# Optimization experiments

Hardware: AMD Instinct MI355X
Metric: run time of the kernel (lower is better)

The kernel has to match this reference:

```python
import jax, jax.numpy as jnp
import numpy as np

B = 131072          # points on manifold
A = 16              # n_anchors
SDIM = 512          # substrate.n (spatial dim); ambient dim = SDIM + 1
ALPHA = 0.1         # attraction coefficient
EPS = 1e-7


def _proj(p):
    # Project onto hyperboloid: recompute time coord from spatial part.
    sp = p[..., 1:]
    t = jnp.sqrt(1.0 + jnp.sum(sp * sp, axis=-1, keepdims=True))
    return jnp.concatenate([t, sp], axis=-1)


def _linner(x, y):
    # Lorentz inner product <x,y>_L = -x0*y0 + sum_i xi*yi
    return -x[..., 0] * y[..., 0] + jnp.sum(x[..., 1:] * y[..., 1:], axis=-1)


def setup_inputs() -> dict:
    key = jax.random.key(0)
    k1, k2 = jax.random.split(key)
    x_sp = jax.random.normal(k1, (B, SDIM), dtype=jnp.float32)
    x = _proj(jnp.concatenate([jnp.zeros((B, 1), jnp.float32), x_sp], axis=-1))
    a_sp = jax.random.normal(k2, (A, SDIM), dtype=jnp.float32) * 0.01
    anchors = _proj(jnp.concatenate([jnp.zeros((A, 1), jnp.float32), a_sp], axis=-1))
    return {"x": x, "anchors": anchors}


def reference(x, anchors):
    af = _proj(anchors)                                   # [A, D]
    D = af.shape[-1]
    metric = jnp.concatenate([-jnp.ones((1,), x.dtype), jnp.ones((D - 1,), x.dtype)])
    # pairwise -<x,a>_L  -> [B, A]
    theta_all = -jnp.einsum('bd,ad->ba', x * metric, af)
    dists = jnp.arccosh(jnp.clip(theta_all, 1.0 + EPS, None))
    idx = jnp.argmin(dists, axis=1)                       # nearest anchor per point
    y = af[idx]                                           # [B, D]
    # log_map_x(y) = acosh(theta)/sqrt(theta^2-1) * (y - theta*x)
    theta = jnp.clip(-_linner(x, y), 1.0 + EPS, None)[:, None]
    direction = (jnp.arccosh(theta) / jnp.sqrt(theta * theta - 1.0)) * (y - theta * x)
    v = ALPHA * direction                                 # tangent vector
    # exp_map_x(v) = cosh(||v||_L) x + sinh(||v||_L)/||v||_L * v
    vn = jnp.sqrt(jnp.clip(_linner(v, v), EPS, None))[:, None]
    return jnp.cosh(vn) * x + (jnp.sinh(vn) / vn) * v
```

## Files before the change

kernel.cpp:

```cpp
#include <hip/hip_runtime.h>

#define NA 16
#define DD 513
#define ALPHA 0.1f
#define EPSV 1e-7f
#define TPW 4
#define GRID 1024

typedef __fp16 h2v __attribute__((ext_vector_type(2)));
typedef __fp16 f16x8 __attribute__((ext_vector_type(8)));
typedef float f32x4 __attribute__((ext_vector_type(4)));
typedef float f32x4u __attribute__((ext_vector_type(4), aligned(4)));
typedef unsigned int u32;

union H2U { h2v h; u32 u; };
union FU  { float f; u32 u; int i; };
union FRAG { u32 w[4]; f16x8 v; };
union U4   { uint4 v; u32 w[4]; };

static __device__ __forceinline__ u32 pkrtz(float lo, float hi) {
    H2U t; t.h = __builtin_amdgcn_cvt_pkrtz(lo, hi); return t.u;
}
static __device__ __forceinline__ h2v asH2(u32 w) { H2U t; t.u = w; return t.h; }

struct __attribute__((packed, aligned(4))) F4 { float x, y, z, w; };


__global__ __launch_bounds__(256, 3)
void hfield_kernel(const float* __restrict__ x,
                   const float* __restrict__ anc,
                   float* __restrict__ out) {
    __shared__ uint4 bframe[NA * 64];
    __shared__ uint4 xframe[4][8 * 64];

    const int tid = threadIdx.x, lane = tid & 63, wid = tid >> 6;
    const int col = lane & 15, g = lane >> 4;

    const int rowbase0 = (blockIdx.x * 4 + wid) * (8 * TPW);
    const float* xb = x + (size_t)rowbase0 * DD;
    uint4* xf = xframe[wid];

    F4 nvA[8], nvB[8];
#pragma unroll
    for (int r = 0; r < 8; ++r) {
        const float* p = xb + (size_t)r * DD + 1 + 4 * lane;
        nvA[r] = *(const F4*)p;
        nvB[r] = *(const F4*)(p + 256);
    }
    __builtin_amdgcn_sched_barrier(0);

#pragma unroll
    for (int m = 0; m < 4; ++m) {
        const int i = m * 256 + tid;
        const int a = i >> 6, u = i & 63;
        const float* p = anc + a * DD + 1 + 4 * u;
        const float* q = p + 256;
        uint4 w;
        w.x = pkrtz(p[0], p[1]);
        w.y = pkrtz(p[2], p[3]);
        w.z = pkrtz(q[0], q[1]);
        w.w = pkrtz(q[2], q[3]);
        bframe[a * 64 + (u ^ (a & 7))] = w;
    }

    float af0c;
    {
        const float* p = anc + col * DD + 1 + g * 128;
        float s = 0.f;
#pragma unroll 16
        for (int i = 0; i < 128; ++i) s = fmaf(p[i], p[i], s);
        s += __shfl_xor(s, 16);
        s += __shfl_xor(s, 32);
        af0c = sqrtf(1.0f + s);
    }
    __syncthreads();

    const float thmin = 1.0f + 1e-7f;

#pragma unroll 1
    for (int t = 0; t < TPW; ++t) {
        const int rowbase = rowbase0 + t * 8;

#pragma unroll
        for (int r = 0; r < 8; ++r) {
            uint4 w;
            w.x = pkrtz(nvA[r].x, nvA[r].y);
            w.y = pkrtz(nvA[r].z, nvA[r].w);
            w.z = pkrtz(nvB[r].x, nvB[r].y);
            w.w = pkrtz(nvB[r].z, nvB[r].w);
            xf[r * 64 + (lane ^ (r & 7))] = w;
        }

        if (t + 1 < TPW) {
            const float* nb = xb + (size_t)((t + 1) * 8) * DD;
#pragma unroll
            for (int r = 0; r < 8; ++r) {
                const float* p = nb + (size_t)r * DD + 1 + 4 * lane;
                nvA[r] = *(const F4*)p;
                nvB[r] = *(const F4*)(p + 256);
            }
            __builtin_amdgcn_sched_barrier(0);
        }

        float x0r[4];
#pragma unroll
        for (int r4 = 0; r4 < 4; ++r4)
            x0r[r4] = xb[(size_t)(t * 8 + ((4 * g + r4) & 7)) * DD];

        f32x4 acc = {0.f, 0.f, 0.f, 0.f};
#pragma unroll
        for (int kt = 0; kt < 16; ++kt) {
            const int u = 4 * kt + g;
            FRAG A, B;
            U4 ax, bx;
            ax.v = xf[(col & 7) * 64 + (u ^ (col & 7))];
            bx.v = bframe[col * 64 + (u ^ (col & 7))];
            A.w[0] = ax.w[0]; A.w[1] = ax.w[1]; A.w[2] = ax.w[2]; A.w[3] = ax.w[3];
            B.w[0] = bx.w[0]; B.w[1] = bx.w[1]; B.w[2] = bx.w[2]; B.w[3] = bx.w[3];
            acc = __builtin_amdgcn_mfma_f32_16x16x32_f16(A.v, B.v, acc, 0, 0, 0);
        }

        float c1r[4], c2r[4], o0r[4];
        int bir[4];
#pragma unroll
        for (int r4 = 0; r4 < 4; ++r4) {
            const float th = fmaxf(fmaf(x0r[r4], af0c, -acc[r4]), thmin);
            FU u; u.f = th;
            u32 key = (u.u & 0xFFFFFFF0u) | (u32)col;
#pragma unroll
            for (int m = 1; m <= 8; m <<= 1) {
                const u32 o = (u32)__shfl_xor((int)key, m);
                key = o < key ? o : key;
            }
            const int bi  = (int)(key & 15u);
            const int src = (lane & 48) | bi;
            const float thw = __shfl(th, src);
            const float y0  = __shfl(af0c, src);

            const float s2 = thw * thw - 1.0f;
            const float rr = sqrtf(s2);
            const float ac = __logf(thw + rr);
            const float cf = ac / rr;
            const float vn = sqrtf(fmaxf(ALPHA * ALPHA * ac * ac, EPSV));
            const float e  = __expf(vn);
            const float ei = 1.0f / e;
            const float ch = 0.5f * (e + ei);
            const float sh = 0.5f * (e - ei);
            const float c2 = ALPHA * cf * (sh / vn);
            const float c1 = fmaf(-c2, thw, ch);

            c1r[r4] = c1;
            c2r[r4] = c2;
            o0r[r4] = fmaf(c2, y0, c1 * x0r[r4]);
            bir[r4] = bi;
        }

#pragma unroll
        for (int r = 0; r < 8; ++r) {
            const int src = (r >> 2) * 16;
            const float c1 = __shfl(c1r[r & 3], src);
            const float c2 = __shfl(c2r[r & 3], src);
            const float o0 = __shfl(o0r[r & 3], src);
            const int   bi = __builtin_amdgcn_readfirstlane(__shfl(bir[r & 3], src));

            U4 X, Y;
            X.v = xf[r * 64 + (lane ^ (r & 7))];
            Y.v = bframe[bi * 64 + (lane ^ (bi & 7))];

            f32x4u s0, s1;
#pragma unroll
            for (int q = 0; q < 2; ++q) {
                const h2v hx = asH2(X.w[q]);
                const h2v hy = asH2(Y.w[q]);
                s0[2 * q]     = fmaf(c2, (float)hy.x, c1 * (float)hx.x);
                s0[2 * q + 1] = fmaf(c2, (float)hy.y, c1 * (float)hx.y);
            }
#pragma unroll
            for (int q = 0; q < 2; ++q) {
                const h2v hx = asH2(X.w[2 + q]);
                const h2v hy = asH2(Y.w[2 + q]);
                s1[2 * q]     = fmaf(c2, (float)hy.x, c1 * (float)hx.x);
                s1[2 * q + 1] = fmaf(c2, (float)hy.y, c1 * (float)hx.y);
            }
            float* op = out + (size_t)(rowbase + r) * DD;
            __builtin_nontemporal_store(s0, (f32x4u*)(op + 1 + 4 * lane));
            __builtin_nontemporal_store(s1, (f32x4u*)(op + 257 + 4 * lane));
            if (lane == 0) __builtin_nontemporal_store(o0, op);
        }
    }
}

extern "C" void kernel_launch(void* const* d_in, const int* in_sizes, int n_in,
                              void* d_out, int out_size, void* d_ws, size_t ws_size,
                              hipStream_t stream) {
    const float* x   = (const float*)d_in[0];
    const float* anc = (const float*)d_in[1];
    float* out       = (float*)d_out;
    hipLaunchKernelGGL(hfield_kernel, dim3(GRID), dim3(256), 0, stream, x, anc, out);
}
```

Baseline: 103.9 us.

## Use FP8 MFMA for anchor distances and keep x in fp16 registers

Switches the x·anchor dot product from fp16 16x16x32 MFMA to fp8 MFMA, storing both x and the anchors (anchors pre-scaled by 16) as packed fp8 in LDS, which halves LDS footprint and read traffic. The output combine now reads x from fp16 values held in registers and the anchor from fp8 LDS. Occupancy hint rises from 3 to 4 blocks, and the next-tile prefetch moves after the output stores, which reduces overlap of loads with compute. FP8 lowers accuracy in both argmin selection and the output's anchor term, so nearest-anchor choices may differ and tolerances may be exceeded.

```diff
diff --git a/kernel.cpp b/kernel.cpp
--- a/kernel.cpp
+++ b/kernel.cpp
@@ -8,37 +8,41 @@
 #define GRID 1024
 
 typedef __fp16 h2v __attribute__((ext_vector_type(2)));
-typedef __fp16 f16x8 __attribute__((ext_vector_type(8)));
+typedef float f32x2 __attribute__((ext_vector_type(2)));
 typedef float f32x4 __attribute__((ext_vector_type(4)));
 typedef float f32x4u __attribute__((ext_vector_type(4), aligned(4)));
 typedef unsigned int u32;
 
 union H2U { h2v h; u32 u; };
 union FU  { float f; u32 u; int i; };
-union FRAG { u32 w[4]; f16x8 v; };
-union U4   { uint4 v; u32 w[4]; };
+union U2L { uint2 v; long l; };
 
 static __device__ __forceinline__ u32 pkrtz(float lo, float hi) {
     H2U t; t.h = __builtin_amdgcn_cvt_pkrtz(lo, hi); return t.u;
 }
 static __device__ __forceinline__ h2v asH2(u32 w) { H2U t; t.u = w; return t.h; }
+static __device__ __forceinline__ u32 pk8(float a, float b, float c, float d) {
+    int w = __builtin_amdgcn_cvt_pk_fp8_f32(a, b, 0, false);
+    w = __builtin_amdgcn_cvt_pk_fp8_f32(c, d, w, true);
+    return (u32)w;
+}
 
 struct __attribute__((packed, aligned(4))) F4 { float x, y, z, w; };
 
 
-__global__ __launch_bounds__(256, 3)
+__global__ __launch_bounds__(256, 4)
 void hfield_kernel(const float* __restrict__ x,
                    const float* __restrict__ anc,
                    float* __restrict__ out) {
-    __shared__ uint4 bframe[NA * 64];
-    __shared__ uint4 xframe[4][8 * 64];
+    __shared__ uint2 bframe[NA * 64];
+    __shared__ uint2 xframe[4][8 * 64];
 
     const int tid = threadIdx.x, lane = tid & 63, wid = tid >> 6;
     const int col = lane & 15, g = lane >> 4;
 
     const int rowbase0 = (blockIdx.x * 4 + wid) * (8 * TPW);
     const float* xb = x + (size_t)rowbase0 * DD;
-    uint4* xf = xframe[wid];
+    uint2* xf = xframe[wid];
 
     F4 nvA[8], nvB[8];
 #pragma unroll
@@ -52,15 +56,13 @@
 #pragma unroll
     for (int m = 0; m < 4; ++m) {
         const int i = m * 256 + tid;
-        const int a = i >> 6, u = i & 63;
-        const float* p = anc + a * DD + 1 + 4 * u;
-        const float* q = p + 256;
-        uint4 w;
-        w.x = pkrtz(p[0], p[1]);
-        w.y = pkrtz(p[2], p[3]);
-        w.z = pkrtz(q[0], q[1]);
-        w.w = pkrtz(q[2], q[3]);
-        bframe[a * 64 + (u ^ (a & 7))] = w;
+        const int a = i >> 6, p = i & 63;
+        const float* s = anc + a * DD + 1 + 4 * p;
+        const float* q = s + 256;
+        uint2 w;
+        w.x = pk8(s[0] * 16.f, s[1] * 16.f, s[2] * 16.f, s[3] * 16.f);
+        w.y = pk8(q[0] * 16.f, q[1] * 16.f, q[2] * 16.f, q[3] * 16.f);
+        bframe[a * 64 + (p ^ a)] = w;
     }
 
     float af0c;
@@ -81,25 +83,17 @@
     for (int t = 0; t < TPW; ++t) {
         const int rowbase = rowbase0 + t * 8;
 
+        u32 xq[8][4];
 #pragma unroll
         for (int r = 0; r < 8; ++r) {
-            uint4 w;
-            w.x = pkrtz(nvA[r].x, nvA[r].y);
-            w.y = pkrtz(nvA[r].z, nvA[r].w);
-            w.z = pkrtz(nvB[r].x, nvB[r].y);
-            w.w = pkrtz(nvB[r].z, nvB[r].w);
-            xf[r * 64 + (lane ^ (r & 7))] = w;
-        }
-
-        if (t + 1 < TPW) {
-            const float* nb = xb + (size_t)((t + 1) * 8) * DD;
-#pragma unroll
-            for (int r = 0; r < 8; ++r) {
-                const float* p = nb + (size_t)r * DD + 1 + 4 * lane;
-                nvA[r] = *(const F4*)p;
-                nvB[r] = *(const F4*)(p + 256);
-            }
-            __builtin_amdgcn_sched_barrier(0);
+            uint2 w;
+            w.x = pk8(nvA[r].x, nvA[r].y, nvA[r].z, nvA[r].w);
+            w.y = pk8(nvB[r].x, nvB[r].y, nvB[r].z, nvB[r].w);
+            xf[r * 64 + (lane ^ (2 * r))] = w;
+            xq[r][0] = pkrtz(nvA[r].x, nvA[r].y);
+            xq[r][1] = pkrtz(nvA[r].z, nvA[r].w);
+            xq[r][2] = pkrtz(nvB[r].x, nvB[r].y);
+            xq[r][3] = pkrtz(nvB[r].z, nvB[r].w);
         }
 
         float x0r[4];
@@ -110,21 +104,18 @@
         f32x4 acc = {0.f, 0.f, 0.f, 0.f};
 #pragma unroll
         for (int kt = 0; kt < 16; ++kt) {
-            const int u = 4 * kt + g;
-            FRAG A, B;
-            U4 ax, bx;
-            ax.v = xf[(col & 7) * 64 + (u ^ (col & 7))];
-            bx.v = bframe[col * 64 + (u ^ (col & 7))];
-            A.w[0] = ax.w[0]; A.w[1] = ax.w[1]; A.w[2] = ax.w[2]; A.w[3] = ax.w[3];
-            B.w[0] = bx.w[0]; B.w[1] = bx.w[1]; B.w[2] = bx.w[2]; B.w[3] = bx.w[3];
-            acc = __builtin_amdgcn_mfma_f32_16x16x32_f16(A.v, B.v, acc, 0, 0, 0);
+            const int p = 4 * kt + g;
+            U2L A, B;
+            A.v = xf[(col & 7) * 64 + (p ^ (2 * (col & 7)))];
+            B.v = bframe[col * 64 + (p ^ col)];
+            acc = __builtin_amdgcn_mfma_f32_16x16x32_fp8_fp8(A.l, B.l, acc, 0, 0, 0);
         }
 
         float c1r[4], c2r[4], o0r[4];
         int bir[4];
 #pragma unroll
         for (int r4 = 0; r4 < 4; ++r4) {
-            const float th = fmaxf(fmaf(x0r[r4], af0c, -acc[r4]), thmin);
+            const float th = fmaxf(fmaf(x0r[r4], af0c, -acc[r4] * 0.0625f), thmin);
             FU u; u.f = th;
             u32 key = (u.u & 0xFFFFFFF0u) | (u32)col;
 #pragma unroll
@@ -162,30 +153,43 @@
             const float c2 = __shfl(c2r[r & 3], src);
             const float o0 = __shfl(o0r[r & 3], src);
             const int   bi = __builtin_amdgcn_readfirstlane(__shfl(bir[r & 3], src));
-
-            U4 X, Y;
-            X.v = xf[r * 64 + (lane ^ (r & 7))];
-            Y.v = bframe[bi * 64 + (lane ^ (bi & 7))];
+            const float c2s = c2 * 0.0625f;
+
+            const uint2 yw = bframe[bi * 64 + (lane ^ bi)];
+            const f32x2 ylo0 = __builtin_amdgcn_cvt_pk_f32_fp8((int)yw.x, false);
+            const f32x2 ylo1 = __builtin_amdgcn_cvt_pk_f32_fp8((int)yw.x, true);
+            const f32x2 yhi0 = __builtin_amdgcn_cvt_pk_f32_fp8((int)yw.y, false);
+            const f32x2 yhi1 = __builtin_amdgcn_cvt_pk_f32_fp8((int)yw.y, true);
+
+            const h2v xa = asH2(xq[r][0]);
+            const h2v xb2 = asH2(xq[r][1]);
+            const h2v xc = asH2(xq[r][2]);
+            const h2v xd = asH2(xq[r][3]);
 
             f32x4u s0, s1;
-#pragma unroll
-            for (int q = 0; q < 2; ++q) {
-                const h2v hx = asH2(X.w[q]);
-                const h2v hy = asH2(Y.w[q]);
-                s0[2 * q]     = fmaf(c2, (float)hy.x, c1 * (float)hx.x);
-                s0[2 * q + 1] = fmaf(c2, (float)hy.y, c1 * (float)hx.y);
-            }
-#pragma unroll
-            for (int q = 0; q < 2; ++q) {
-                const h2v hx = asH2(X.w[2 + q]);
-                const h2v hy = asH2(Y.w[2 + q]);
-                s1[2 * q]     = fmaf(c2, (float)hy.x, c1 * (float)hx.x);
-                s1[2 * q + 1] = fmaf(c2, (float)hy.y, c1 * (float)hx.y);
-            }
+            s0[0] = fmaf(c2s, ylo0.x, c1 * (float)xa.x);
+            s0[1] = fmaf(c2s, ylo0.y, c1 * (float)xa.y);
+            s0[2] = fmaf(c2s, ylo1.x, c1 * (float)xb2.x);
+            s0[3] = fmaf(c2s, ylo1.y, c1 * (float)xb2.y);
+            s1[0] = fmaf(c2s, yhi0.x, c1 * (float)xc.x);
+            s1[1] = fmaf(c2s, yhi0.y, c1 * (float)xc.y);
+            s1[2] = fmaf(c2s, yhi1.x, c1 * (float)xd.x);
+            s1[3] = fmaf(c2s, yhi1.y, c1 * (float)xd.y);
+
             float* op = out + (size_t)(rowbase + r) * DD;
             __builtin_nontemporal_store(s0, (f32x4u*)(op + 1 + 4 * lane));
             __builtin_nontemporal_store(s1, (f32x4u*)(op + 257 + 4 * lane));
             if (lane == 0) __builtin_nontemporal_store(o0, op);
+        }
+
+        if (t + 1 < TPW) {
+            const float* nb = xb + (size_t)((t + 1) * 8) * DD;
+#pragma unroll
+            for (int r = 0; r < 8; ++r) {
+                const float* p = nb + (size_t)r * DD + 1 + 4 * lane;
+                nvA[r] = *(const F4*)p;
+                nvB[r] = *(const F4*)(p + 256);
+            }
         }
     }
 }
```

Result: slower. 147.2 us (+41.7%).
